# Kernel optimization log

Hardware: AMD Instinct MI355X
Metric: run time of the kernel (lower is better)

## Reference

```python
import jax, jax.numpy as jnp
import numpy as np

H, D = 8, 32          # num_heads, head dim (hidden = 256)
HID = H * D
LRELU = 0.2
NT, NC, E, FIN = 60000, 30000, 200000, 64


def setup_inputs() -> dict:
    key = jax.random.key(0)
    ks = jax.random.split(key, 24)
    s = 0.05
    inp = {
        'x_trans': jax.random.normal(ks[0], (NT, FIN), jnp.float32),
        'x_cc':    jax.random.normal(ks[1], (NC, FIN), jnp.float32),
        'src_c2t': jax.random.randint(ks[2], (E,), 0, NC),
        'dst_c2t': jax.random.randint(ks[3], (E,), 0, NT),
        'src_t2c': jax.random.randint(ks[4], (E,), 0, NT),
        'dst_t2c': jax.random.randint(ks[5], (E,), 0, NC),
        'W_in': jax.random.normal(ks[6], (2, FIN, HID), jnp.float32) * s,
        'b_in': jnp.zeros((2, HID), jnp.float32),
        'Wk': jax.random.normal(ks[7], (2, 2, HID, HID), jnp.float32) * s,
        'bk': jnp.zeros((2, 2, HID), jnp.float32),
        'Wq': jax.random.normal(ks[8], (2, 2, HID, HID), jnp.float32) * s,
        'bq': jnp.zeros((2, 2, HID), jnp.float32),
        'Wv': jax.random.normal(ks[9], (2, 2, HID, HID), jnp.float32) * s,
        'bv': jnp.zeros((2, 2, HID), jnp.float32),
        'Wa': jax.random.normal(ks[10], (2, 2, HID, HID), jnp.float32) * s,
        'ba': jnp.zeros((2, 2, HID), jnp.float32),
        'a_rel': jax.random.normal(ks[11], (2, 2, H, D, D), jnp.float32) * s,
        'm_rel': jax.random.normal(ks[12], (2, 2, H, D, D), jnp.float32) * s,
        'p_rel': jnp.ones((2, 2, H), jnp.float32),
        'skip':  jnp.ones((2, 2), jnp.float32),
        'W_out': jax.random.normal(ks[13], (HID, 64), jnp.float32) * s,
        'b_out': jnp.zeros((64,), jnp.float32),
    }
    return inp


def _hgt_layer(xs, Wk, bk, Wq, bq, Wv, bv, Wa, ba, a_rel, m_rel, p_rel, skip, edges):
    # xs: list of [N_t, HID] per node type; edges: list of (src_type, dst_type, src_idx, dst_idx)
    nt = len(xs)
    k = [(xs[t] @ Wk[t] + bk[t]).reshape(-1, H, D) for t in range(nt)]
    q = [(xs[t] @ Wq[t] + bq[t]).reshape(-1, H, D) for t in range(nt)]
    v = [(xs[t] @ Wv[t] + bv[t]).reshape(-1, H, D) for t in range(nt)]
    agg = [jnp.zeros((xs[t].shape[0], H, D), xs[t].dtype) for t in range(nt)]
    inv_sqrt_d = 1.0 / jnp.sqrt(jnp.float32(D))
    for r, (st, dt, si, di) in enumerate(edges):
        kr = jnp.einsum('nhd,hde->nhe', k[st], a_rel[r])   # relation-transformed keys
        vr = jnp.einsum('nhd,hde->nhe', v[st], m_rel[r])   # relation-transformed messages
        ke, ve, qe = kr[si], vr[si], q[dt][di]             # [E, H, D] gathers
        alpha = jnp.einsum('ehd,ehd->eh', qe, ke) * p_rel[r] * inv_sqrt_d  # [E, H]
        n_dst = xs[dt].shape[0]
        m = jax.ops.segment_max(alpha, di, num_segments=n_dst)
        ex = jnp.exp(alpha - m[di])
        ssum = jax.ops.segment_sum(ex, di, num_segments=n_dst)
        w = ex / (ssum[di] + 1e-16)                         # segment softmax per dst node
        agg[dt] = agg[dt] + jax.ops.segment_sum(ve * w[..., None], di, num_segments=n_dst)
    out = []
    for t in range(nt):
        o = jax.nn.gelu(agg[t].reshape(-1, HID), approximate=False)
        o = o @ Wa[t] + ba[t]
        beta = jax.nn.sigmoid(skip[t])
        out.append(beta * o + (1.0 - beta) * xs[t])
    return out


def reference(x_trans, x_cc, src_c2t, dst_c2t, src_t2c, dst_t2c,
              W_in, b_in, Wk, bk, Wq, bq, Wv, bv, Wa, ba,
              a_rel, m_rel, p_rel, skip, W_out, b_out):
    # per-node-type Linear + in-place relu
    xs = [jax.nn.relu(x_trans @ W_in[0] + b_in[0]),
          jax.nn.relu(x_cc @ W_in[1] + b_in[1])]
    # relation 0: cc_node -> trans_node ; relation 1: trans_node -> cc_node
    edges = [(1, 0, src_c2t, dst_c2t), (0, 1, src_t2c, dst_t2c)]
    n_layers = Wk.shape[0]
    for l in range(n_layers):
        xs = _hgt_layer(xs, Wk[l], bk[l], Wq[l], bq[l], Wv[l], bv[l], Wa[l], ba[l],
                        a_rel[l], m_rel[l], p_rel[l], skip[l], edges)
    # dropout is identity in eval mode
    y = xs[0] @ W_out + b_out
    y = jnp.where(y > 0, y, LRELU * y)                      # LeakyReLU(0.2)
    n = jnp.linalg.norm(y, axis=1, keepdims=True)
    return y / jnp.maximum(n, 1e-12)                        # F.normalize(p=2, dim=1)
```

## Files before the change

### kernel.cpp

```cpp
#include <hip/hip_runtime.h>
#include <hip/hip_bf16.h>
#include <math.h>

#define NTN 60000
#define NCN 30000
#define NED 200000

typedef unsigned short u16;
typedef unsigned long long u64;
typedef __attribute__((ext_vector_type(8))) u16 u16x8;
typedef __attribute__((ext_vector_type(8))) __bf16 bf16x8;
typedef __attribute__((ext_vector_type(4))) float f32x4;

static __device__ __forceinline__ float bf2f(u16 u) {
    return __uint_as_float(((unsigned)u) << 16);
}
static __device__ __forceinline__ u16 f2bf(float f) {
    unsigned u = __float_as_uint(f);
    unsigned r = (u + 0x7fffu + ((u >> 16) & 1u)) >> 16;
    return (u16)r;
}

__global__ void fill2(unsigned* __restrict__ a, int na, unsigned* __restrict__ b, int nb) {
    int i = blockIdx.x * blockDim.x + threadIdx.x;
    int st = gridDim.x * blockDim.x;
    for (int k = i; k < na; k += st) a[k] = 0u;
    for (int k = i; k < nb; k += st) b[k] = 0u;
}

__global__ void f32_to_bf16(const float* __restrict__ in, u16* __restrict__ out, int n4) {
    int i = blockIdx.x * blockDim.x + threadIdx.x;
    int stride = gridDim.x * blockDim.x;
    for (; i < n4; i += stride) {
        float4 v = ((const float4*)in)[i];
        ushort4 o;
        o.x = f2bf(v.x); o.y = f2bf(v.y); o.z = f2bf(v.z); o.w = f2bf(v.w);
        ((ushort4*)out)[i] = o;
    }
}

__global__ void convTb(const float* __restrict__ in, u16* __restrict__ out,
                       int K, int N, int inStride, int outStride, int nm) {
    int idx = blockIdx.x * blockDim.x + threadIdx.x;
    int per = N * (K >> 2);
    int total = per * nm;
    if (idx >= total) return;
    int mat = idx / per, rem = idx - mat * per;
    int k4 = rem / N, n = rem - k4 * N;
    int k = k4 * 4;
    const float* src = in + (size_t)mat * inStride;
    u16* dst = out + (size_t)mat * outStride;
    ushort4 o;
    o.x = f2bf(src[(size_t)(k + 0) * N + n]);
    o.y = f2bf(src[(size_t)(k + 1) * N + n]);
    o.z = f2bf(src[(size_t)(k + 2) * N + n]);
    o.w = f2bf(src[(size_t)(k + 3) * N + n]);
    *(ushort4*)(dst + (size_t)n * K + k) = o;
}

__global__ void copy_bq(const float* __restrict__ bq, float* __restrict__ bqkv) {
    int lt = blockIdx.x;
    bqkv[lt * 768 + threadIdx.x] = bq[lt * 256 + threadIdx.x];
}

__global__ __launch_bounds__(256) void fuse_weights(
    const float* __restrict__ Wk, const float* __restrict__ bk,
    const float* __restrict__ Wv, const float* __restrict__ bv,
    const float* __restrict__ a_rel, const float* __restrict__ m_rel,
    const float* __restrict__ p_rel,
    float* __restrict__ Wf2, float* __restrict__ bqkv)
{
    __shared__ float kw[256], vw[256];
    const int c = blockIdx.x, lt = blockIdx.y, tid = threadIdx.x;
    const int l = lt >> 1, t = lt & 1;
    const int lr = l * 2 + (t == 1 ? 0 : 1);
    const float* WkP = Wk + (size_t)lt * 65536;
    const float* WvP = Wv + (size_t)lt * 65536;
    const float* ar = a_rel + (size_t)lr * 8192;
    const float* mr = m_rel + (size_t)lr * 8192;
    kw[tid] = WkP[c * 256 + tid];
    vw[tid] = WvP[c * 256 + tid];
    __syncthreads();
    const int h = tid >> 5, e = tid & 31;
    const float s = p_rel[lr * 8 + h] * 0.17677669529663687f;
    float ak = 0.f, av = 0.f;
#pragma unroll 8
    for (int d = 0; d < 32; ++d) {
        ak += kw[h * 32 + d] * ar[h * 1024 + d * 32 + e];
        av += vw[h * 32 + d] * mr[h * 1024 + d * 32 + e];
    }
    float* WkfP = Wf2 + (size_t)lt * 131072;
    WkfP[c * 256 + tid] = ak * s;
    WkfP[65536 + c * 256 + tid] = av;
    if (c == 0) {
        const float* bkP = bk + (size_t)lt * 256;
        const float* bvP = bv + (size_t)lt * 256;
        float bka = 0.f, bva = 0.f;
#pragma unroll 8
        for (int d = 0; d < 32; ++d) {
            bka += bkP[h * 32 + d] * ar[h * 1024 + d * 32 + e];
            bva += bvP[h * 32 + d] * mr[h * 1024 + d * 32 + e];
        }
        bqkv[lt * 768 + 256 + tid] = bka * s;
        bqkv[lt * 768 + 512 + tid] = bva;
    }
}

template <int EPI, int BN, bool OBF, int KT>
__global__ __launch_bounds__(256) void gemm_mfma2(
    int nblk0,
    const u16* __restrict__ A0, const u16* __restrict__ W0, const float* __restrict__ b0,
    void* __restrict__ C0, int M0, int ldC0, int NY0,
    const u16* __restrict__ xr0, const float* __restrict__ sk0,
    const u16* __restrict__ A1, const u16* __restrict__ W1, const float* __restrict__ b1,
    void* __restrict__ C1, int M1, int ldC1, int NY1,
    const u16* __restrict__ xr1, const float* __restrict__ sk1)
{
    constexpr int ASZ = 64 * 64;
    constexpr int BSZ = BN * 64;
    constexpr int NF = BN / 32;
    constexpr int NT = KT >> 6;
    __shared__ u16 smem[2 * (ASZ + BSZ)];
    u16* Abuf[2] = {smem, smem + ASZ + BSZ};
    u16* Bbuf[2] = {smem + ASZ, smem + ASZ + BSZ + ASZ};

    const int nwg = gridDim.x;
    const int bid = blockIdx.x;
    const int q8 = nwg >> 3, r8 = nwg & 7;
    const int xcd = bid & 7, pos = bid >> 3;
    const int lbid = (xcd < r8) ? xcd * (q8 + 1) + pos
                                : r8 * (q8 + 1) + (xcd - r8) * q8 + pos;

    const u16* A; const u16* WT; const float* bias; void* Cv;
    int M, ldC, NY, sb; const u16* xres; const float* skipPtr;
    if (lbid < nblk0) {
        A = A0; WT = W0; bias = b0; Cv = C0; M = M0; ldC = ldC0; NY = NY0;
        xres = xr0; skipPtr = sk0; sb = lbid;
    } else {
        A = A1; WT = W1; bias = b1; Cv = C1; M = M1; ldC = ldC1; NY = NY1;
        xres = xr1; skipPtr = sk1; sb = lbid - nblk0;
    }
    const int bx = sb / NY, by = sb - bx * NY;
    const int m0 = bx * 64, n0 = by * BN;

    const int tid = threadIdx.x;
    const int wave = tid >> 6, lane = tid & 63;
    const int wm = (wave >> 1) * 32, wn = (wave & 1) * (BN / 2);
    f32x4 acc[2][NF];
#pragma unroll
    for (int i = 0; i < 2; ++i)
#pragma unroll
        for (int j = 0; j < NF; ++j) acc[i][j] = (f32x4){0.f, 0.f, 0.f, 0.f};

    const int sr = lane >> 3;
    const int sl = lane & 7;

    const u16* gpa[2];
    const u16* gpb[NF];
#pragma unroll
    for (int i = 0; i < 2; ++i) {
        int r = wave * 16 + i * 8 + sr;
        int gr = m0 + r; gr = gr < M ? gr : M - 1;
        gpa[i] = A + (size_t)gr * KT + ((sl ^ sr) << 3);
    }
#pragma unroll
    for (int i = 0; i < NF; ++i) {
        int r = wave * (BN / 4) + i * 8 + sr;
        gpb[i] = WT + (size_t)(n0 + r) * KT + ((sl ^ sr) << 3);
    }

    auto stage = [&](int k0, u16* Ad, u16* Bd) {
#pragma unroll
        for (int i = 0; i < 2; ++i) {
            int rb = wave * 16 + i * 8;
            __builtin_amdgcn_global_load_lds(
                (const __attribute__((address_space(1))) void*)(gpa[i] + k0),
                (__attribute__((address_space(3))) void*)(Ad + rb * 64), 16, 0, 0);
        }
#pragma unroll
        for (int i = 0; i < NF; ++i) {
            int rb = wave * (BN / 4) + i * 8;
            __builtin_amdgcn_global_load_lds(
                (const __attribute__((address_space(1))) void*)(gpb[i] + k0),
                (__attribute__((address_space(3))) void*)(Bd + rb * 64), 16, 0, 0);
        }
    };

    auto compute = [&](const u16* Ab, const u16* Bb) {
#pragma unroll
        for (int kx = 0; kx < 2; ++kx) {
            bf16x8 af[2], bfr[NF];
#pragma unroll
            for (int mf = 0; mf < 2; ++mf) {
                int r = wm + mf * 16 + (lane & 15);
                int slot = (lane >> 4) + kx * 4;
                af[mf] = __builtin_bit_cast(bf16x8,
                    *(const u16x8*)(Ab + r * 64 + ((slot ^ (r & 7)) << 3)));
            }
#pragma unroll
            for (int nf = 0; nf < NF; ++nf) {
                int r = wn + nf * 16 + (lane & 15);
                int slot = (lane >> 4) + kx * 4;
                bfr[nf] = __builtin_bit_cast(bf16x8,
                    *(const u16x8*)(Bb + r * 64 + ((slot ^ (r & 7)) << 3)));
            }
#pragma unroll
            for (int mf = 0; mf < 2; ++mf)
#pragma unroll
                for (int nf = 0; nf < NF; ++nf)
                    acc[mf][nf] = __builtin_amdgcn_mfma_f32_16x16x32_bf16(
                        af[mf], bfr[nf], acc[mf][nf], 0, 0, 0);
        }
    };

    stage(0, Abuf[0], Bbuf[0]);
#pragma unroll
    for (int t = 0; t < NT; ++t) {
        const int pb = t & 1;
        if (t + 1 < NT) {
            stage((t + 1) << 6, Abuf[pb ^ 1], Bbuf[pb ^ 1]);
            __builtin_amdgcn_sched_barrier(0);
            if constexpr (BN == 128) asm volatile("s_waitcnt vmcnt(6)" ::: "memory");
            else                     asm volatile("s_waitcnt vmcnt(4)" ::: "memory");
        } else {
            asm volatile("s_waitcnt vmcnt(0)" ::: "memory");
        }
        __builtin_amdgcn_s_barrier();
        __builtin_amdgcn_sched_barrier(0);
        compute(Abuf[pb], Bbuf[pb]);
        __builtin_amdgcn_sched_barrier(0);
        __builtin_amdgcn_s_barrier();
        __builtin_amdgcn_sched_barrier(0);
    }

    float beta = 0.f;
    if (EPI == 2) beta = 1.f / (1.f + expf(-skipPtr[0]));

    if constexpr (OBF) {
        constexpr int CLD = BN + 12;
        u16* Ct = smem;
#pragma unroll
        for (int nf = 0; nf < NF; ++nf) {
            int col = wn + nf * 16 + (lane & 15);
            int gcol = n0 + col;
            float bs = bias[gcol];
#pragma unroll
            for (int mf = 0; mf < 2; ++mf) {
#pragma unroll
                for (int j = 0; j < 4; ++j) {
                    int row = wm + mf * 16 + (lane >> 4) * 4 + j;
                    int grow = m0 + row;
                    int gr2 = grow < M ? grow : 0;
                    float c = acc[mf][nf][j] + bs;
                    if (EPI == 1) c = fmaxf(c, 0.f);
                    if (EPI == 2) c = beta * c + (1.f - beta) * bf2f(xres[(size_t)gr2 * ldC + gcol]);
                    if (EPI == 3) c = (c > 0.f) ? c : 0.2f * c;
                    Ct[row * CLD + col] = f2bf(c);
                }
            }
        }
        __syncthreads();
        int row = tid >> 2, c0 = (tid & 3) * (BN / 4);
        int grow = m0 + row;
        if (grow < M) {
            u16* dst = (u16*)Cv + (size_t)grow * ldC + n0 + c0;
            const u16* src = Ct + row * CLD + c0;
#pragma unroll
            for (int i = 0; i < BN / 32; ++i)
                *(u16x8*)(dst + i * 8) = *(const u16x8*)(src + i * 8);
        }
    } else {
#pragma unroll
        for (int nf = 0; nf < NF; ++nf) {
            int gcol = n0 + wn + nf * 16 + (lane & 15);
            float bs = bias[gcol];
#pragma unroll
            for (int mf = 0; mf < 2; ++mf) {
#pragma unroll
                for (int j = 0; j < 4; ++j) {
                    int grow = m0 + wm + mf * 16 + (lane >> 4) * 4 + j;
                    if (grow >= M) continue;
                    float c = acc[mf][nf][j] + bs;
                    if (EPI == 1) c = fmaxf(c, 0.f);
                    if (EPI == 3) c = (c > 0.f) ? c : 0.2f * c;
                    ((float*)Cv)[(size_t)grow * ldC + gcol] = c;
                }
            }
        }
    }
}

__global__ void hist2(const int* __restrict__ d0, unsigned* __restrict__ c0,
                      const int* __restrict__ d1, unsigned* __restrict__ c1, int E) {
    int e = blockIdx.x * blockDim.x + threadIdx.x;
    if (e < E) {
        atomicAdd(&c0[d0[e]], 1u);
        atomicAdd(&c1[d1[e]], 1u);
    }
}

__global__ __launch_bounds__(256) void scan_blocks2(
    const unsigned* __restrict__ c0, unsigned* __restrict__ p0, unsigned* __restrict__ bs0, int N0,
    const unsigned* __restrict__ c1, unsigned* __restrict__ p1, unsigned* __restrict__ bs1, int N1)
{
    const unsigned* counts = blockIdx.y ? c1 : c0;
    unsigned* pref = blockIdx.y ? p1 : p0;
    unsigned* bsum = blockIdx.y ? bs1 : bs0;
    int N = blockIdx.y ? N1 : N0;
    if ((int)blockIdx.x * 256 >= N) return;
    __shared__ unsigned tmp[256];
    int i = blockIdx.x * 256 + threadIdx.x;
    unsigned v = (i < N) ? counts[i] : 0u;
    tmp[threadIdx.x] = v;
    __syncthreads();
    for (int off = 1; off < 256; off <<= 1) {
        unsigned t = (threadIdx.x >= off) ? tmp[threadIdx.x - off] : 0u;
        __syncthreads();
        tmp[threadIdx.x] += t;
        __syncthreads();
    }
    if (i < N) pref[i] = tmp[threadIdx.x] - v;
    if (threadIdx.x == 255) bsum[blockIdx.x] = tmp[255];
}

__global__ __launch_bounds__(256) void scan_top2(
    unsigned* __restrict__ bs0, int NB0, unsigned* __restrict__ bs1, int NB1)
{
    unsigned* bsum = blockIdx.x ? bs1 : bs0;
    int NB = blockIdx.x ? NB1 : NB0;
    __shared__ unsigned tmp[256];
    unsigned v = ((int)threadIdx.x < NB) ? bsum[threadIdx.x] : 0u;
    tmp[threadIdx.x] = v;
    __syncthreads();
    for (int off = 1; off < 256; off <<= 1) {
        unsigned t = (threadIdx.x >= off) ? tmp[threadIdx.x - off] : 0u;
        __syncthreads();
        tmp[threadIdx.x] += t;
        __syncthreads();
    }
    if ((int)threadIdx.x < NB) bsum[threadIdx.x] = tmp[threadIdx.x] - v;
}

__global__ void scan_add2(
    const unsigned* __restrict__ p0, const unsigned* __restrict__ bs0,
    const unsigned* __restrict__ c0, unsigned* __restrict__ cur0, u64* __restrict__ ri0, int N0,
    const unsigned* __restrict__ p1, const unsigned* __restrict__ bs1,
    const unsigned* __restrict__ c1, unsigned* __restrict__ cur1, u64* __restrict__ ri1, int N1)
{
    const unsigned* pref = blockIdx.y ? p1 : p0;
    const unsigned* bsum = blockIdx.y ? bs1 : bs0;
    const unsigned* counts = blockIdx.y ? c1 : c0;
    unsigned* cursor = blockIdx.y ? cur1 : cur0;
    u64* rowinfo = blockIdx.y ? ri1 : ri0;
    int N = blockIdx.y ? N1 : N0;
    int i = blockIdx.x * 256 + threadIdx.x;
    if (i < N) {
        unsigned s = pref[i] + bsum[blockIdx.x];
        cursor[i] = s;
        rowinfo[i] = (u64)s | ((u64)counts[i] << 32);
    }
}

__global__ void place2(const int* __restrict__ d0, const int* __restrict__ s0,
                       unsigned* __restrict__ cur0, unsigned* __restrict__ o0,
                       const int* __restrict__ d1, const int* __restrict__ s1,
                       unsigned* __restrict__ cur1, unsigned* __restrict__ o1, int E) {
    int e = blockIdx.x * blockDim.x + threadIdx.x;
    if (e < E) {
        unsigned p = atomicAdd(&cur0[d0[e]], 1u);
        o0[p] = (unsigned)s0[e] * 768u;
        unsigned q = atomicAdd(&cur1[d1[e]], 1u);
        o1[q] = (unsigned)s1[e] * 768u;
    }
}

#define TBLK8 ((NTN + 7) / 8)
__global__ __launch_bounds__(256) void edge_gather2(
    const u16* __restrict__ qkvT, const u16* __restrict__ qkvC,
    const u64* __restrict__ riT, const unsigned* __restrict__ srcT,
    const u64* __restrict__ riC, const unsigned* __restrict__ srcC,
    u16* __restrict__ aggT, u16* __restrict__ aggC)
{
    const int b = blockIdx.x;
    const bool isT = b < TBLK8;
    const int lane = threadIdx.x & 63;
    const int lq = lane & 31;
    const int n = (((isT ? b : b - TBLK8) << 2) + (int)(threadIdx.x >> 6)) * 2 + (lane >> 5);

    const u16* qkv_d = isT ? qkvT : qkvC;
    const u16* qkv_s = isT ? qkvC : qkvT;
    const u64* ri = isT ? riT : riC;
    const unsigned* srcarr = isT ? srcT : srcC;
    u16* agg = isT ? aggT : aggC;

    const u64 rinfo = ri[n];
    const unsigned start = (unsigned)rinfo;
    const unsigned deg = (unsigned)(rinfo >> 32);
    u16* outp = &agg[(size_t)n * 256 + lq * 8];

    if (deg == 0) {
        *(u16x8*)outp = (u16x8){0, 0, 0, 0, 0, 0, 0, 0};
        return;
    }

    u16x8 qv = *(const u16x8*)&qkv_d[(size_t)n * 768 + lq * 8];
    float qf[8];
#pragma unroll
    for (int i = 0; i < 8; ++i) qf[i] = bf2f(qv[i]);

    const u16* kvb = qkv_s + 256 + lq * 8;
    float m = -INFINITY, s = 0.f;
    float acc[8] = {0.f, 0.f, 0.f, 0.f, 0.f, 0.f, 0.f, 0.f};

    unsigned off = srcarr[start];
    u16x8 kr = *(const u16x8*)(kvb + off);
    u16x8 vr = *(const u16x8*)(kvb + off + 256);
    for (unsigned j = 0;;) {
        const bool more = (j + 1 < deg);
        u16x8 kr_n, vr_n;
        if (more) {
            unsigned off2 = srcarr[start + j + 1];
            kr_n = *(const u16x8*)(kvb + off2);
            vr_n = *(const u16x8*)(kvb + off2 + 256);
        }
        float kf[8];
#pragma unroll
        for (int i = 0; i < 8; ++i) kf[i] = bf2f(kr[i]);
        float p = qf[0] * kf[0] + qf[1] * kf[1] + qf[2] * kf[2] + qf[3] * kf[3]
                + qf[4] * kf[4] + qf[5] * kf[5] + qf[6] * kf[6] + qf[7] * kf[7];
        p += __shfl_xor(p, 1);
        p += __shfl_xor(p, 2);
        float vf[8];
#pragma unroll
        for (int i = 0; i < 8; ++i) vf[i] = bf2f(vr[i]);
        if (__ballot(p > m) == 0ull) {
            float wv = __expf(p - m);
            s += wv;
#pragma unroll
            for (int i = 0; i < 8; ++i) acc[i] += wv * vf[i];
        } else {
            float mn = fmaxf(m, p);
            float sc = __expf(m - mn);
            float wv = __expf(p - mn);
            s = s * sc + wv;
#pragma unroll
            for (int i = 0; i < 8; ++i) acc[i] = acc[i] * sc + wv * vf[i];
            m = mn;
        }
        if (!more) break;
        kr = kr_n; vr = vr_n; ++j;
    }

    float inv = 1.f / (s + 1e-16f);
    u16x8 ov;
#pragma unroll
    for (int i = 0; i < 8; ++i) {
        float x = acc[i] * inv;
        float y2 = 1.5957691216f * x + 0.0713548163f * x * x * x;
        float e = __expf(y2);
        float t = 1.f - 2.f / (e + 1.f);
        ov[i] = f2bf(0.5f * x * (1.f + t));
    }
    *(u16x8*)outp = ov;
}

__global__ __launch_bounds__(256) void norm_rows(float* __restrict__ y, int M) {
    int row = blockIdx.x * 4 + (threadIdx.x >> 6);
    int lane = threadIdx.x & 63;
    if (row >= M) return;
    float v = y[(size_t)row * 64 + lane];
    float s = v * v;
#pragma unroll
    for (int off = 1; off < 64; off <<= 1) s += __shfl_xor(s, off);
    float n = sqrtf(s);
    y[(size_t)row * 64 + lane] = v / fmaxf(n, 1e-12f);
}

extern "C" void kernel_launch(void* const* d_in, const int* in_sizes, int n_in,
                              void* d_out, int out_size, void* d_ws, size_t ws_size,
                              hipStream_t stream)
{
    const float* x_trans = (const float*)d_in[0];
    const float* x_cc    = (const float*)d_in[1];
    const int* src_c2t   = (const int*)d_in[2];
    const int* dst_c2t   = (const int*)d_in[3];
    const int* src_t2c   = (const int*)d_in[4];
    const int* dst_t2c   = (const int*)d_in[5];
    const float* W_in = (const float*)d_in[6];
    const float* b_in = (const float*)d_in[7];
    const float* Wk   = (const float*)d_in[8];
    const float* bk   = (const float*)d_in[9];
    const float* Wq   = (const float*)d_in[10];
    const float* bq   = (const float*)d_in[11];
    const float* Wv   = (const float*)d_in[12];
    const float* bv   = (const float*)d_in[13];
    const float* Wa   = (const float*)d_in[14];
    const float* ba   = (const float*)d_in[15];
    const float* a_rel = (const float*)d_in[16];
    const float* m_rel = (const float*)d_in[17];
    const float* p_rel = (const float*)d_in[18];
    const float* skip  = (const float*)d_in[19];
    const float* W_out = (const float*)d_in[20];
    const float* b_out = (const float*)d_in[21];

    char* w = (char*)d_ws;
    auto alloc = [&](size_t bytes) { char* p = w; w += (bytes + 255) & ~(size_t)255; return p; };
    u16* xs0  = (u16*)alloc((size_t)NTN * 256 * 2);
    u16* xs1  = (u16*)alloc((size_t)NCN * 256 * 2);
    u16* xin0 = (u16*)alloc((size_t)NTN * 64 * 2);
    u16* xin1 = (u16*)alloc((size_t)NCN * 64 * 2);
    u16* qkv0 = (u16*)alloc((size_t)NTN * 768 * 2);
    u16* qkv1 = (u16*)alloc((size_t)NCN * 768 * 2);
    u16* agg0 = (u16*)alloc((size_t)NTN * 256 * 2);
    u16* agg1 = (u16*)alloc((size_t)NCN * 256 * 2);
    u16* WinT = (u16*)alloc((size_t)2 * 16384 * 2);
    u16* WqkvT= (u16*)alloc((size_t)4 * 196608 * 2);
    u16* WaT  = (u16*)alloc((size_t)4 * 65536 * 2);
    u16* WoutT= (u16*)alloc((size_t)16384 * 2);
    float* Wf2 = (float*)alloc((size_t)4 * 131072 * 4);
    float* bqkv = (float*)alloc((size_t)4 * 768 * 4);
    unsigned* countsT   = (unsigned*)alloc((size_t)NTN * 4);
    unsigned* prefT     = (unsigned*)alloc((size_t)NTN * 4);
    unsigned* cursorT   = (unsigned*)alloc((size_t)NTN * 4);
    u64* rowinfoT       = (u64*)alloc((size_t)NTN * 8);
    unsigned* srcAT     = (unsigned*)alloc((size_t)NED * 4);
    unsigned* countsC   = (unsigned*)alloc((size_t)NCN * 4);
    unsigned* prefC     = (unsigned*)alloc((size_t)NCN * 4);
    unsigned* cursorC   = (unsigned*)alloc((size_t)NCN * 4);
    u64* rowinfoC       = (u64*)alloc((size_t)NCN * 8);
    unsigned* srcAC     = (unsigned*)alloc((size_t)NED * 4);
    unsigned* bsum      = (unsigned*)alloc((size_t)2 * 256 * 4);
    (void)ws_size; (void)in_sizes; (void)n_in; (void)out_size;

    {
        const int EB = (NED + 255) / 256;
        const int NBt = (NTN + 255) / 256, NBc = (NCN + 255) / 256;
        fill2<<<256, 256, 0, stream>>>(countsT, NTN, countsC, NCN);
        hist2<<<EB, 256, 0, stream>>>(dst_c2t, countsT, dst_t2c, countsC, NED);
        scan_blocks2<<<dim3(NBt, 2), 256, 0, stream>>>(countsT, prefT, bsum, NTN,
                                                       countsC, prefC, bsum + 256, NCN);
        scan_top2<<<2, 256, 0, stream>>>(bsum, NBt, bsum + 256, NBc);
        scan_add2<<<dim3(NBt, 2), 256, 0, stream>>>(
            prefT, bsum, countsT, cursorT, rowinfoT, NTN,
            prefC, bsum + 256, countsC, cursorC, rowinfoC, NCN);
        place2<<<EB, 256, 0, stream>>>(dst_c2t, src_c2t, cursorT, srcAT,
                                       dst_t2c, src_t2c, cursorC, srcAC, NED);
    }

    fuse_weights<<<dim3(256, 4), 256, 0, stream>>>(Wk, bk, Wv, bv, a_rel, m_rel, p_rel, Wf2, bqkv);
    copy_bq<<<4, 256, 0, stream>>>(bq, bqkv);
    convTb<<<(4 * 16384 + 255) / 256, 256, 0, stream>>>(Wq, WqkvT, 256, 256, 65536, 196608, 4);
    convTb<<<(4 * 16384 + 255) / 256, 256, 0, stream>>>(Wf2, WqkvT + 65536, 256, 256, 131072, 196608, 4);
    convTb<<<(4 * 16384 + 255) / 256, 256, 0, stream>>>(Wf2 + 65536, WqkvT + 131072, 256, 256, 131072, 196608, 4);
    convTb<<<(4 * 16384 + 255) / 256, 256, 0, stream>>>(Wa, WaT, 256, 256, 65536, 65536, 4);
    convTb<<<(2 * 4096 + 255) / 256, 256, 0, stream>>>(W_in, WinT, 64, 256, 16384, 16384, 2);
    convTb<<<(4096 + 255) / 256, 256, 0, stream>>>(W_out, WoutT, 256, 64, 16384, 16384, 1);
    f32_to_bf16<<<1024, 256, 0, stream>>>(x_trans, xin0, NTN * 64 / 4);
    f32_to_bf16<<<1024, 256, 0, stream>>>(x_cc,    xin1, NCN * 64 / 4);

    const int GT = (NTN + 63) / 64, GC = (NCN + 63) / 64;

    gemm_mfma2<1, 64, true, 64><<<GT * 4 + GC * 4, 256, 0, stream>>>(
        GT * 4,
        xin0, WinT, b_in, xs0, NTN, 256, 4, nullptr, nullptr,
        xin1, WinT + 16384, b_in + 256, xs1, NCN, 256, 4, nullptr, nullptr);

    for (int l = 0; l < 2; ++l) {
        size_t lt0 = (size_t)(l * 2 + 0), lt1 = (size_t)(l * 2 + 1);

        gemm_mfma2<0, 64, true, 256><<<GT * 12 + GC * 12, 256, 0, stream>>>(
            GT * 12,
            xs0, WqkvT + lt0 * 196608, bqkv + lt0 * 768, qkv0, NTN, 768, 12, nullptr, nullptr,
            xs1, WqkvT + lt1 * 196608, bqkv + lt1 * 768, qkv1, NCN, 768, 12, nullptr, nullptr);

        edge_gather2<<<TBLK8 + (NCN + 7) / 8, 256, 0, stream>>>(
            qkv0, qkv1,
            rowinfoT, srcAT,
            rowinfoC, srcAC,
            agg0, agg1);

        gemm_mfma2<2, 64, true, 256><<<GT * 4 + GC * 4, 256, 0, stream>>>(
            GT * 4,
            agg0, WaT + lt0 * 65536, ba + lt0 * 256, xs0, NTN, 256, 4, xs0, skip + l * 2 + 0,
            agg1, WaT + lt1 * 65536, ba + lt1 * 256, xs1, NCN, 256, 4, xs1, skip + l * 2 + 1);
    }

    {
        float* y = (float*)d_out;
        gemm_mfma2<3, 64, false, 256><<<GT, 256, 0, stream>>>(
            GT,
            xs0, WoutT, b_out, y, NTN, 64, 1, nullptr, nullptr,
            xs0, WoutT, b_out, y, NTN, 64, 1, nullptr, nullptr);
        norm_rows<<<NTN / 4, 256, 0, stream>>>(y, NTN);
    }
}
```

Baseline: 475.1 us.

## Triple-buffer GEMM LDS pipeline and batch small conversion kernels into fewer launches

The bf16 MFMA GEMM moves from double to triple buffering in LDS, keeping two K-tiles of global-to-LDS loads in flight. The vmcnt wait counts are derived from the loads still outstanding. Four weight-transpose launches are merged into one 2D-grid kernel, and the two input f32-to-bf16 conversions share one launch, to cut launch overhead. The cost is 1.5x shared memory per block, which may reduce occupancy, and the K=64 GEMM (one tile) gains nothing.

```diff
diff --git a/kernel.cpp b/kernel.cpp
--- a/kernel.cpp
+++ b/kernel.cpp
@@ -28,14 +28,21 @@
     for (int k = i; k < nb; k += st) b[k] = 0u;
 }
 
-__global__ void f32_to_bf16(const float* __restrict__ in, u16* __restrict__ out, int n4) {
+__global__ void f32_to_bf16_2(const float* __restrict__ in0, u16* __restrict__ out0, int n40,
+                              const float* __restrict__ in1, u16* __restrict__ out1, int n41) {
     int i = blockIdx.x * blockDim.x + threadIdx.x;
     int stride = gridDim.x * blockDim.x;
-    for (; i < n4; i += stride) {
-        float4 v = ((const float4*)in)[i];
+    for (int k = i; k < n40; k += stride) {
+        float4 v = ((const float4*)in0)[k];
         ushort4 o;
         o.x = f2bf(v.x); o.y = f2bf(v.y); o.z = f2bf(v.z); o.w = f2bf(v.w);
-        ((ushort4*)out)[i] = o;
+        ((ushort4*)out0)[k] = o;
+    }
+    for (int k = i; k < n41; k += stride) {
+        float4 v = ((const float4*)in1)[k];
+        ushort4 o;
+        o.x = f2bf(v.x); o.y = f2bf(v.y); o.z = f2bf(v.z); o.w = f2bf(v.w);
+        ((ushort4*)out1)[k] = o;
     }
 }
 
@@ -56,6 +63,32 @@
     o.z = f2bf(src[(size_t)(k + 2) * N + n]);
     o.w = f2bf(src[(size_t)(k + 3) * N + n]);
     *(ushort4*)(dst + (size_t)n * K + k) = o;
+}
+
+__global__ void convT4(const float* __restrict__ s0, u16* __restrict__ d0, int is0, int os0,
+                       const float* __restrict__ s1, u16* __restrict__ d1, int is1, int os1,
+                       const float* __restrict__ s2, u16* __restrict__ d2, int is2, int os2,
+                       const float* __restrict__ s3, u16* __restrict__ d3, int is3, int os3) {
+    const float* in; u16* out; int inStride, outStride;
+    switch (blockIdx.y) {
+        case 0: in = s0; out = d0; inStride = is0; outStride = os0; break;
+        case 1: in = s1; out = d1; inStride = is1; outStride = os1; break;
+        case 2: in = s2; out = d2; inStride = is2; outStride = os2; break;
+        default: in = s3; out = d3; inStride = is3; outStride = os3; break;
+    }
+    int idx = blockIdx.x * blockDim.x + threadIdx.x;
+    const int per = 256 * 64;
+    int mat = idx / per, rem = idx - mat * per;
+    int k4 = rem >> 8, n = rem & 255;
+    int k = k4 * 4;
+    const float* src = in + (size_t)mat * inStride;
+    u16* dst = out + (size_t)mat * outStride;
+    ushort4 o;
+    o.x = f2bf(src[(size_t)(k + 0) * 256 + n]);
+    o.y = f2bf(src[(size_t)(k + 1) * 256 + n]);
+    o.z = f2bf(src[(size_t)(k + 2) * 256 + n]);
+    o.w = f2bf(src[(size_t)(k + 3) * 256 + n]);
+    *(ushort4*)(dst + (size_t)n * 256 + k) = o;
 }
 
 __global__ void copy_bq(const float* __restrict__ bq, float* __restrict__ bqkv) {
@@ -120,9 +153,8 @@
     constexpr int BSZ = BN * 64;
     constexpr int NF = BN / 32;
     constexpr int NT = KT >> 6;
-    __shared__ u16 smem[2 * (ASZ + BSZ)];
-    u16* Abuf[2] = {smem, smem + ASZ + BSZ};
-    u16* Bbuf[2] = {smem + ASZ, smem + ASZ + BSZ + ASZ};
+    constexpr int L = 2 + NF;
+    __shared__ u16 smem[3 * (ASZ + BSZ)];
 
     const int nwg = gridDim.x;
     const int bid = blockIdx.x;
@@ -169,7 +201,10 @@
         gpb[i] = WT + (size_t)(n0 + r) * KT + ((sl ^ sr) << 3);
     }
 
-    auto stage = [&](int k0, u16* Ad, u16* Bd) {
+    auto stage = [&](int t, int buf) {
+        const int k0 = t << 6;
+        u16* Ad = smem + buf * (ASZ + BSZ);
+        u16* Bd = Ad + ASZ;
 #pragma unroll
         for (int i = 0; i < 2; ++i) {
             int rb = wave * 16 + i * 8;
@@ -186,7 +221,9 @@
         }
     };
 
-    auto compute = [&](const u16* Ab, const u16* Bb) {
+    auto compute = [&](int buf) {
+        const u16* Ab = smem + buf * (ASZ + BSZ);
+        const u16* Bb = Ab + ASZ;
 #pragma unroll
         for (int kx = 0; kx < 2; ++kx) {
             bf16x8 af[2], bfr[NF];
@@ -213,21 +250,24 @@
         }
     };
 
-    stage(0, Abuf[0], Bbuf[0]);
+    stage(0, 0);
+    if constexpr (NT >= 2) stage(1, 1);
 #pragma unroll
     for (int t = 0; t < NT; ++t) {
-        const int pb = t & 1;
-        if (t + 1 < NT) {
-            stage((t + 1) << 6, Abuf[pb ^ 1], Bbuf[pb ^ 1]);
+        if (t + 2 < NT) {
+            stage(t + 2, (t + 2) % 3);
             __builtin_amdgcn_sched_barrier(0);
-            if constexpr (BN == 128) asm volatile("s_waitcnt vmcnt(6)" ::: "memory");
-            else                     asm volatile("s_waitcnt vmcnt(4)" ::: "memory");
-        } else {
-            asm volatile("s_waitcnt vmcnt(0)" ::: "memory");
-        }
+        }
+        const int rem = NT - 1 - t;
+        const int wc = (rem >= 2) ? 2 * L : rem * L;
+        if (wc == 0)       asm volatile("s_waitcnt vmcnt(0)" ::: "memory");
+        else if (wc == 4)  asm volatile("s_waitcnt vmcnt(4)" ::: "memory");
+        else if (wc == 6)  asm volatile("s_waitcnt vmcnt(6)" ::: "memory");
+        else if (wc == 8)  asm volatile("s_waitcnt vmcnt(8)" ::: "memory");
+        else               asm volatile("s_waitcnt vmcnt(12)" ::: "memory");
         __builtin_amdgcn_s_barrier();
         __builtin_amdgcn_sched_barrier(0);
-        compute(Abuf[pb], Bbuf[pb]);
+        compute(t % 3);
         __builtin_amdgcn_sched_barrier(0);
         __builtin_amdgcn_s_barrier();
         __builtin_amdgcn_sched_barrier(0);
@@ -549,14 +589,15 @@
 
     fuse_weights<<<dim3(256, 4), 256, 0, stream>>>(Wk, bk, Wv, bv, a_rel, m_rel, p_rel, Wf2, bqkv);
     copy_bq<<<4, 256, 0, stream>>>(bq, bqkv);
-    convTb<<<(4 * 16384 + 255) / 256, 256, 0, stream>>>(Wq, WqkvT, 256, 256, 65536, 196608, 4);
-    convTb<<<(4 * 16384 + 255) / 256, 256, 0, stream>>>(Wf2, WqkvT + 65536, 256, 256, 131072, 196608, 4);
-    convTb<<<(4 * 16384 + 255) / 256, 256, 0, stream>>>(Wf2 + 65536, WqkvT + 131072, 256, 256, 131072, 196608, 4);
-    convTb<<<(4 * 16384 + 255) / 256, 256, 0, stream>>>(Wa, WaT, 256, 256, 65536, 65536, 4);
+    convT4<<<dim3(256, 4), 256, 0, stream>>>(
+        Wq, WqkvT, 65536, 196608,
+        Wf2, WqkvT + 65536, 131072, 196608,
+        Wf2 + 65536, WqkvT + 131072, 131072, 196608,
+        Wa, WaT, 65536, 65536);
     convTb<<<(2 * 4096 + 255) / 256, 256, 0, stream>>>(W_in, WinT, 64, 256, 16384, 16384, 2);
     convTb<<<(4096 + 255) / 256, 256, 0, stream>>>(W_out, WoutT, 256, 64, 16384, 16384, 1);
-    f32_to_bf16<<<1024, 256, 0, stream>>>(x_trans, xin0, NTN * 64 / 4);
-    f32_to_bf16<<<1024, 256, 0, stream>>>(x_cc,    xin1, NCN * 64 / 4);
+    f32_to_bf16_2<<<1024, 256, 0, stream>>>(x_trans, xin0, NTN * 64 / 4,
+                                            x_cc, xin1, NCN * 64 / 4);
 
     const int GT = (NTN + 63) / 64, GC = (NCN + 63) / 64;
 
```

Result: slower. 485.5 us (+2.2%).
